# Kernel optimization log

Hardware: AMD Instinct MI355X
Metric: run time of the kernel (lower is better)

The kernel has to match this reference:

```python
import jax, jax.numpy as jnp
import numpy as np

GRID_SIZE = 5
SPLINE_ORDER = 3
INPUT_DIM = 4096
BATCH = 4096
N_BASIS = GRID_SIZE + SPLINE_ORDER - 1  # 7


def _extended_knots():
    # Uniform grid on [-1, 1] extended by spline_order knots on each side so the
    # Cox-de Boor recursion is well defined (the original torch code indexes
    # grid[i+k+1] past the end; this is the standard intended knot extension).
    grid = np.linspace(-1.0, 1.0, GRID_SIZE)
    h = grid[1] - grid[0]
    left = grid[0] - h * np.arange(SPLINE_ORDER, 0, -1)
    right = grid[-1] + h * np.arange(1, SPLINE_ORDER + 1)
    return jnp.asarray(np.concatenate([left, grid, right]), dtype=jnp.float32)  # (11,)


def _bspline_basis(x, knots):
    # x: (B, D) -> basis: (B, D, N_BASIS), fully vectorized Cox-de Boor recursion.
    t = knots
    xe = x[..., None]                                   # (B, D, 1)
    Bk = ((xe >= t[:-1]) & (xe < t[1:])).astype(x.dtype)  # degree 0: (B, D, 10)
    for k in range(1, SPLINE_ORDER + 1):
        n = t.shape[0] - k - 1
        left = (xe - t[:n]) / (t[k:k + n] - t[:n]) * Bk[..., :n]
        right = (t[k + 1:k + 1 + n] - xe) / (t[k + 1:k + 1 + n] - t[1:1 + n]) * Bk[..., 1:n + 1]
        Bk = left + right
    return Bk  # (B, D, 7)


def setup_inputs() -> dict:
    key = jax.random.key(0)
    kx, kc = jax.random.split(key)
    x = jax.random.uniform(kx, (BATCH, INPUT_DIM), dtype=jnp.float32, minval=-1.0, maxval=1.0)
    coeffs = jax.random.normal(kc, (INPUT_DIM, N_BASIS), dtype=jnp.float32)
    return {"x": x, "coeffs": coeffs}


def reference(x, coeffs):
    knots = _extended_knots()
    basis = _bspline_basis(x, knots)          # (B, D, K)
    return jnp.einsum('bdk,dk->bd', basis, coeffs)
```

## Files before the change

### kernel.cpp

```cpp
#include <hip/hip_runtime.h>


typedef float f4v __attribute__((ext_vector_type(4)));

#define D     4096
#define B     4096
#define NB    7
#define DTILE 256
#define ROWS  64

constexpr int NDT    = D / DTILE;
constexpr int NRT    = B / ROWS;
constexpr int STRIDE = 20;

__global__ __launch_bounds__(256, 4) void
spline_act_kernel(const float* __restrict__ x,
                  const float* __restrict__ coeffs,
                  float* __restrict__ out) {
    __shared__ float sc[DTILE * STRIDE];
    __shared__ float raw[DTILE * NB];

    const int bid   = blockIdx.x;
    const int dt    = bid & (NDT - 1);
    const int rowt  = bid >> 4;
    const int dbase = dt * DTILE;
    const int t     = threadIdx.x;

    {
        const f4v* c4 = reinterpret_cast<const f4v*>(coeffs + (size_t)dbase * NB);
        f4v* r4 = reinterpret_cast<f4v*>(raw);
        r4[t] = c4[t];
        if (t < (DTILE * NB / 4) - 256)
            r4[256 + t] = c4[256 + t];
        __syncthreads();

        const int dl = 4 * (t & 63) + (t >> 6);
        float cr[NB];
#pragma unroll
        for (int k = 0; k < NB; ++k) cr[k] = raw[dl * NB + k];

        const float k6 = 1.0f / 6.0f;
        float* bp = &sc[t * STRIDE];
#pragma unroll
        for (int c = 0; c < 4; ++c) {
            float A  = cr[c];
            float Bv = cr[c + 1];
            float C  = cr[c + 2];
            float Dv = cr[c + 3];
            f4v p;
            p[0] = (A + 4.0f * Bv + C) * k6;
            p[1] = (C - A) * 0.5f;
            p[2] = (A + C) * 0.5f - Bv;
            p[3] = (Dv - A + 3.0f * (Bv - C)) * k6;
            *reinterpret_cast<f4v*>(bp + 4 * c) = p;
        }
        __syncthreads();
    }

    const int pos  = t & 63;
    const int rsub = t >> 6;
    const int lbase = pos * STRIDE;

    const f4v* x4 = reinterpret_cast<const f4v*>(x);
    f4v*       o4 = reinterpret_cast<f4v*>(out);

    const int rstep = 4 * (D / 4);
    int idx = (rowt * ROWS + rsub) * (D / 4) + (dbase >> 2) + pos;

    auto process = [&](f4v xv, int iidx) {
        f4v r;
#pragma unroll
        for (int j = 0; j < 4; ++j) {
            float u  = fmaf(xv[j], 2.0f, 2.0f);
            float cf = floorf(u);
            cf = fminf(fmaxf(cf, 0.0f), 3.0f);
            float s  = u - cf;
            int   c  = (int)cf;
            const f4v cv = *reinterpret_cast<const f4v*>(
                &sc[lbase + j * (64 * STRIDE) + (c << 2)]);
            r[j] = fmaf(fmaf(fmaf(cv[3], s, cv[2]), s, cv[1]), s, cv[0]);
        }
        __builtin_nontemporal_store(r, &o4[iidx]);
    };

    f4v a0 = __builtin_nontemporal_load(&x4[idx + 0 * rstep]);
    f4v a1 = __builtin_nontemporal_load(&x4[idx + 1 * rstep]);
    f4v a2 = __builtin_nontemporal_load(&x4[idx + 2 * rstep]);
    f4v a3 = __builtin_nontemporal_load(&x4[idx + 3 * rstep]);

#pragma unroll
    for (int g = 0; g < 4; ++g) {
        f4v b0, b1, b2, b3;
        const int nidx = idx + 4 * rstep;
        if (g < 3) {
            b0 = __builtin_nontemporal_load(&x4[nidx + 0 * rstep]);
            b1 = __builtin_nontemporal_load(&x4[nidx + 1 * rstep]);
            b2 = __builtin_nontemporal_load(&x4[nidx + 2 * rstep]);
            b3 = __builtin_nontemporal_load(&x4[nidx + 3 * rstep]);
        } else {
            b0 = a0; b1 = a1; b2 = a2; b3 = a3;
        }
        process(a0, idx + 0 * rstep);
        process(a1, idx + 1 * rstep);
        process(a2, idx + 2 * rstep);
        process(a3, idx + 3 * rstep);
        a0 = b0; a1 = b1; a2 = b2; a3 = b3;
        idx = nidx;
    }
}

extern "C" void kernel_launch(void* const* d_in, const int* in_sizes, int n_in,
                              void* d_out, int out_size, void* d_ws, size_t ws_size,
                              hipStream_t stream) {
    const float* x      = (const float*)d_in[0];
    const float* coeffs = (const float*)d_in[1];
    float* out          = (float*)d_out;

    const int grid = NDT * NRT;
    spline_act_kernel<<<grid, 256, 0, stream>>>(x, coeffs, out);
}
```

Measured before the change: 119.7 us.

## Halve rows per block, drop raw LDS buffer, raise occupancy to 8 blocks

Halves the rows handled per block, which doubles the grid. The separate raw coefficient buffer is removed and the coefficients are staged in the sc buffer instead, with an extra barrier, so each block uses less LDS. Launch bounds are raised to 8 blocks per CU. The explicit software-pipelined nontemporal loads and stores are replaced by a plain unrolled loop with ordinary loads and stores, trading manual prefetch for more resident waves; the coefficient precompute now runs twice as often overall.

```diff
diff --git a/kernel.cpp b/kernel.cpp
--- a/kernel.cpp
+++ b/kernel.cpp
@@ -7,18 +7,17 @@
 #define B     4096
 #define NB    7
 #define DTILE 256
-#define ROWS  64
+#define ROWS  32
 
 constexpr int NDT    = D / DTILE;
 constexpr int NRT    = B / ROWS;
 constexpr int STRIDE = 20;
 
-__global__ __launch_bounds__(256, 4) void
+__global__ __launch_bounds__(256, 8) void
 spline_act_kernel(const float* __restrict__ x,
                   const float* __restrict__ coeffs,
                   float* __restrict__ out) {
     __shared__ float sc[DTILE * STRIDE];
-    __shared__ float raw[DTILE * NB];
 
     const int bid   = blockIdx.x;
     const int dt    = bid & (NDT - 1);
@@ -28,7 +27,7 @@
 
     {
         const f4v* c4 = reinterpret_cast<const f4v*>(coeffs + (size_t)dbase * NB);
-        f4v* r4 = reinterpret_cast<f4v*>(raw);
+        f4v* r4 = reinterpret_cast<f4v*>(sc);
         r4[t] = c4[t];
         if (t < (DTILE * NB / 4) - 256)
             r4[256 + t] = c4[256 + t];
@@ -37,7 +36,8 @@
         const int dl = 4 * (t & 63) + (t >> 6);
         float cr[NB];
 #pragma unroll
-        for (int k = 0; k < NB; ++k) cr[k] = raw[dl * NB + k];
+        for (int k = 0; k < NB; ++k) cr[k] = sc[dl * NB + k];
+        __syncthreads();
 
         const float k6 = 1.0f / 6.0f;
         float* bp = &sc[t * STRIDE];
@@ -57,17 +57,21 @@
         __syncthreads();
     }
 
-    const int pos  = t & 63;
-    const int rsub = t >> 6;
+    const int pos   = t & 63;
+    const int rsub  = t >> 6;
     const int lbase = pos * STRIDE;
 
     const f4v* x4 = reinterpret_cast<const f4v*>(x);
     f4v*       o4 = reinterpret_cast<f4v*>(out);
 
-    const int rstep = 4 * (D / 4);
-    int idx = (rowt * ROWS + rsub) * (D / 4) + (dbase >> 2) + pos;
+    const int rowbase = rowt * ROWS;
 
-    auto process = [&](f4v xv, int iidx) {
+#pragma unroll
+    for (int it = 0; it < ROWS / 4; ++it) {
+        const int row = rowbase + it * 4 + rsub;
+        const int idx = row * (D / 4) + (dbase >> 2) + pos;
+
+        const f4v xv = x4[idx];
         f4v r;
 #pragma unroll
         for (int j = 0; j < 4; ++j) {
@@ -80,32 +84,7 @@
                 &sc[lbase + j * (64 * STRIDE) + (c << 2)]);
             r[j] = fmaf(fmaf(fmaf(cv[3], s, cv[2]), s, cv[1]), s, cv[0]);
         }
-        __builtin_nontemporal_store(r, &o4[iidx]);
-    };
-
-    f4v a0 = __builtin_nontemporal_load(&x4[idx + 0 * rstep]);
-    f4v a1 = __builtin_nontemporal_load(&x4[idx + 1 * rstep]);
-    f4v a2 = __builtin_nontemporal_load(&x4[idx + 2 * rstep]);
-    f4v a3 = __builtin_nontemporal_load(&x4[idx + 3 * rstep]);
-
-#pragma unroll
-    for (int g = 0; g < 4; ++g) {
-        f4v b0, b1, b2, b3;
-        const int nidx = idx + 4 * rstep;
-        if (g < 3) {
-            b0 = __builtin_nontemporal_load(&x4[nidx + 0 * rstep]);
-            b1 = __builtin_nontemporal_load(&x4[nidx + 1 * rstep]);
-            b2 = __builtin_nontemporal_load(&x4[nidx + 2 * rstep]);
-            b3 = __builtin_nontemporal_load(&x4[nidx + 3 * rstep]);
-        } else {
-            b0 = a0; b1 = a1; b2 = a2; b3 = a3;
-        }
-        process(a0, idx + 0 * rstep);
-        process(a1, idx + 1 * rstep);
-        process(a2, idx + 2 * rstep);
-        process(a3, idx + 3 * rstep);
-        a0 = b0; a1 = b1; a2 = b2; a3 = b3;
-        idx = nidx;
+        o4[idx] = r;
     }
 }
 
```

After: 116.8 us. 1.02x faster.
